# Performance work log

Hardware: AMD Instinct MI355X
Metric: run time of the kernel (lower is better)

Reference implementation:

```python
import jax, jax.numpy as jnp
import numpy as np

B, T, C, H = 8, 2048, 512, 512


def setup_inputs() -> dict:
    key = jax.random.key(0)
    ks = jax.random.split(key, 9)
    s = 1.0 / np.sqrt(C)
    return {
        "q": jax.random.normal(ks[0], (B, T, C), jnp.float32),
        "k": jax.random.normal(ks[1], (B, T, C), jnp.float32),
        "v": jax.random.normal(ks[2], (B, T, C), jnp.float32),
        "Wq": jax.random.normal(ks[3], (C, H), jnp.float32) * s,
        "bq": jax.random.normal(ks[4], (H,), jnp.float32) * 0.01,
        "Wk": jax.random.normal(ks[5], (C, H), jnp.float32) * s,
        "bk": jax.random.normal(ks[6], (H,), jnp.float32) * 0.01,
        "Wv": jax.random.normal(ks[7], (C, H), jnp.float32) * s,
        "bv": jax.random.normal(ks[8], (H,), jnp.float32) * 0.01,
    }


def reference(q, k, v, Wq, bq, Wk, bk, Wv, bv):
    # Linear projections (Real_Linear == nn.Linear): [B,T,C] @ [C,H] + [H]
    query = jnp.einsum('btc,ch->bth', q, Wq) + bq
    key_p = jnp.einsum('btc,ch->bth', k, Wk) + bk
    value = jnp.einsum('btc,ch->bth', v, Wv) + bv
    # energy = Q @ K^T / sqrt(H)  -> [B, T, T]
    energy = jnp.einsum('bth,byh->bty', query, key_p) / jnp.sqrt(jnp.asarray(H, query.dtype))
    attn = jax.nn.softmax(energy, axis=-1)
    # weighted value: [B, T, T] @ [B, T, H] -> [B, T, H]
    return jnp.einsum('bty,byh->bth', attn, value)
```

## Files before the change

### kernel.cpp

```cpp
#include <hip/hip_runtime.h>
#include <hip/hip_bf16.h>

typedef unsigned short u16;
typedef unsigned int u32;
typedef short s16x8 __attribute__((ext_vector_type(8)));
typedef float f32x4 __attribute__((ext_vector_type(4)));

#define NB 8
#define NT 2048
#define NC 512
#define NH 512

__device__ __forceinline__ u16 f2bf(float f) {
  unsigned u = __float_as_uint(f);
  u += 0x7FFFu + ((u >> 16) & 1u);
  return (u16)(u >> 16);
}

__device__ __forceinline__ void gld16(const u16* src, u16* lds_dst) {
  __builtin_amdgcn_global_load_lds(
      (const __attribute__((address_space(1))) u32*)src,
      (__attribute__((address_space(3))) u32*)lds_dst, 16, 0, 0);
}

__global__ __launch_bounds__(256) void wt_kernel(const float* __restrict__ Wq,
                                                 const float* __restrict__ Wk,
                                                 const float* __restrict__ Wv,
                                                 u16* __restrict__ WqT,
                                                 u16* __restrict__ WkT,
                                                 u16* __restrict__ WvT) {
  __shared__ float tile[32][33];
  const float* W = (blockIdx.z == 0) ? Wq : (blockIdx.z == 1) ? Wk : Wv;
  u16* WT = (blockIdx.z == 0) ? WqT : (blockIdx.z == 1) ? WkT : WvT;
  const int x = threadIdx.x & 31;
  const int y = threadIdx.x >> 5;
  const int k0 = blockIdx.x * 32, h0 = blockIdx.y * 32;
#pragma unroll
  for (int p = 0; p < 4; ++p)
    tile[y + 8 * p][x] = W[(size_t)(k0 + y + 8 * p) * NH + h0 + x];
  __syncthreads();
#pragma unroll
  for (int p = 0; p < 4; ++p)
    WT[(size_t)(h0 + y + 8 * p) * NC + k0 + x] = f2bf(tile[x][y + 8 * p]);
}

__global__ __launch_bounds__(256) void proj_kernel(const float* __restrict__ Xq,
                                                   const float* __restrict__ Xk,
                                                   const float* __restrict__ Xv,
                                                   const u16* __restrict__ WqT,
                                                   const u16* __restrict__ WkT,
                                                   const u16* __restrict__ WvT,
                                                   const float* __restrict__ bq,
                                                   const float* __restrict__ bk,
                                                   const float* __restrict__ bv,
                                                   u16* __restrict__ Yq,
                                                   u16* __restrict__ Yk,
                                                   u16* __restrict__ Yv) {
  __shared__ __align__(16) u16 Asub[2][128 * 40];
  __shared__ __align__(16) u16 Bsub[2][128 * 40];
  const int zz = blockIdx.z;
  const float* X = (zz == 0) ? Xq : (zz == 1) ? Xk : Xv;
  const u16* WT = (zz == 0) ? WqT : (zz == 1) ? WkT : WvT;
  const float* bias = (zz == 0) ? bq : (zz == 1) ? bk : bv;
  u16* Y = (zz == 0) ? Yq : (zz == 1) ? Yk : Yv;

  const int t = threadIdx.x;
  const int lane = t & 63;
  const int w = t >> 6;
  const int l16 = lane & 15;
  const int ko8 = (lane >> 4) * 8;
  const int m0 = blockIdx.y * 128;
  const int n0 = blockIdx.x * 128;
  const int wr = (w >> 1) * 64, wc = (w & 1) * 64;
  f32x4 acc[4][4] = {};

  float4 areg[4];
  int4 breg[2];
#define PLOAD(kt)                                                              \
  {                                                                            \
    const int k0_ = (kt) * 32;                                                 \
    _Pragma("unroll")                                                          \
    for (int p = 0; p < 4; ++p) {                                              \
      int c = t + 256 * p;                                                     \
      areg[p] = *(const float4*)&X[(size_t)(m0 + (c >> 3)) * NC + k0_ + (c & 7) * 4]; \
    }                                                                          \
    _Pragma("unroll")                                                          \
    for (int p = 0; p < 2; ++p) {                                              \
      int c = t + 256 * p;                                                     \
      breg[p] = *(const int4*)&WT[(size_t)(n0 + (c >> 2)) * NC + k0_ + (c & 3) * 8];  \
    }                                                                          \
  }
#define PWRITE(buf)                                                            \
  {                                                                            \
    _Pragma("unroll")                                                          \
    for (int p = 0; p < 4; ++p) {                                              \
      int c = t + 256 * p;                                                     \
      ushort4 bb;                                                              \
      bb.x = f2bf(areg[p].x); bb.y = f2bf(areg[p].y);                          \
      bb.z = f2bf(areg[p].z); bb.w = f2bf(areg[p].w);                          \
      *(ushort4*)&Asub[buf][(c >> 3) * 40 + (c & 7) * 4] = bb;                 \
    }                                                                          \
    _Pragma("unroll")                                                          \
    for (int p = 0; p < 2; ++p) {                                              \
      int c = t + 256 * p;                                                     \
      *(int4*)&Bsub[buf][(c >> 2) * 40 + (c & 3) * 8] = breg[p];               \
    }                                                                          \
  }

  PLOAD(0)
  PWRITE(0)
  __syncthreads();

  int pb = 0;
  for (int kt = 0; kt < 16; ++kt) {
    if (kt < 15) PLOAD(kt + 1)
    s16x8 af[4], bf[4];
#pragma unroll
    for (int i = 0; i < 4; ++i)
      af[i] = *(const s16x8*)&Asub[pb][(wr + i * 16 + l16) * 40 + ko8];
#pragma unroll
    for (int j = 0; j < 4; ++j)
      bf[j] = *(const s16x8*)&Bsub[pb][(wc + j * 16 + l16) * 40 + ko8];
#pragma unroll
    for (int i = 0; i < 4; ++i)
#pragma unroll
      for (int j = 0; j < 4; ++j)
        acc[i][j] = __builtin_amdgcn_mfma_f32_16x16x32_bf16(af[i], bf[j], acc[i][j], 0, 0, 0);
    if (kt < 15) PWRITE(pb ^ 1)
    __syncthreads();
    pb ^= 1;
  }
#undef PLOAD
#undef PWRITE
  const int rg = (lane >> 4) * 4;
#pragma unroll
  for (int i = 0; i < 4; ++i)
#pragma unroll
    for (int j = 0; j < 4; ++j) {
      const int col = n0 + wc + j * 16 + l16;
      const float bcol = bias[col];
#pragma unroll
      for (int jj = 0; jj < 4; ++jj) {
        const int row = m0 + wr + i * 16 + rg + jj;
        Y[(size_t)row * NH + col] = f2bf(acc[i][j][jj] + bcol);
      }
    }
}

__global__ __launch_bounds__(256) void vt_kernel(const u16* __restrict__ Vp,
                                                 u16* __restrict__ VpT) {
  __shared__ u16 tile[32][33];
  const int x = threadIdx.x & 31;
  const int y = threadIdx.x >> 5;
  const int t0 = blockIdx.x * 32, h0 = blockIdx.y * 32, b = blockIdx.z;
  const u16* src = Vp + (size_t)b * NT * NH;
  u16* dst = VpT + (size_t)b * NH * NT;
#pragma unroll
  for (int p = 0; p < 4; ++p)
    tile[y + 8 * p][x] = src[(size_t)(t0 + y + 8 * p) * NH + h0 + x];
  __syncthreads();
#pragma unroll
  for (int p = 0; p < 4; ++p)
    dst[(size_t)(h0 + y + 8 * p) * NT + t0 + x] = tile[x][y + 8 * p];
}

__global__ __launch_bounds__(512, 2) void flash_partial(const u16* __restrict__ Qp,
                                                        const u16* __restrict__ Kp,
                                                        const u16* __restrict__ VpT,
                                                        float* __restrict__ O0,
                                                        float* __restrict__ O1,
                                                        float* __restrict__ mlws) {
  __shared__ __align__(16) u16 Klds[2][32 * 512];
  __shared__ __align__(16) u16 Vlds[2][32 * 512];

  const int t = threadIdx.x;
  const int lane = t & 63;
  const int w = t >> 6;
  const int l16 = lane & 15;
  const int g = lane >> 4;
  const int g8 = g * 8;
  const int b = blockIdx.x;
  const int q0 = blockIdx.y * 128;
  const int z = blockIdx.z;
  const int qg = q0 + w * 16 + l16;
  const int kperm = (l16 >> 2) * 8 + (l16 & 3);
  const float kscale = 0.044194173824159216f;

  s16x8 qf[16];
  {
    const u16* qrow = Qp + (size_t)(b * NT + qg) * NH;
#pragma unroll
    for (int ks = 0; ks < 16; ++ks)
      qf[ks] = *(const s16x8*)&qrow[ks * 32 + g8];
  }

  f32x4 oacc[32] = {};
  float m_run = -1e30f, l_run = 0.f;

  const u16* kbat = Kp + (size_t)(b * NT + z * 1024) * NH;
  const u16* vbat = VpT + (size_t)b * NH * NT + z * 1024;

#define STAGE(buf, it)                                                         \
  {                                                                            \
    _Pragma("unroll")                                                          \
    for (int r = 0; r < 4; ++r) {                                              \
      const int i = w * 4 + r;                                      \
                 \
      gld16(kbat + (size_t)((it) * 32 + kperm + ((i & 1) << 2)) * NH           \
                 + ((i >> 1) << 5) + g8,                                       \
            &Klds[buf][i * 512]);                                              \
                                 \
      gld16(vbat + (size_t)(i * 16 + l16) * NT + (it) * 32 + g8,               \
            &Vlds[buf][i * 512]);                                              \
    }                                                                          \
  }

  STAGE(0, 0)
  __syncthreads();

  int pb = 0;
  for (int it = 0; it < 32; ++it) {
    if (it < 31) STAGE(pb ^ 1, it + 1)
    f32x4 s0 = {}, s1 = {};
    __builtin_amdgcn_s_setprio(1);
#pragma unroll
    for (int ks = 0; ks < 16; ++ks) {
      s16x8 kf0 = *(const s16x8*)&Klds[pb][(ks * 2 + 0) * 512 + lane * 8];
      s16x8 kf1 = *(const s16x8*)&Klds[pb][(ks * 2 + 1) * 512 + lane * 8];
      s0 = __builtin_amdgcn_mfma_f32_16x16x32_bf16(kf0, qf[ks], s0, 0, 0, 0);
      s1 = __builtin_amdgcn_mfma_f32_16x16x32_bf16(kf1, qf[ks], s1, 0, 0, 0);
    }
    __builtin_amdgcn_s_setprio(0);
    float pv[8];
#pragma unroll
    for (int j = 0; j < 4; ++j) { pv[j] = s0[j] * kscale; pv[4 + j] = s1[j] * kscale; }
    float mx = pv[0];
#pragma unroll
    for (int j = 1; j < 8; ++j) mx = fmaxf(mx, pv[j]);
    mx = fmaxf(mx, __shfl_xor(mx, 16, 64));
    mx = fmaxf(mx, __shfl_xor(mx, 32, 64));
    if (__any(mx > m_run + 8.f)) {
      const float m_new = fmaxf(m_run, mx);
      const float scale = __expf(m_run - m_new);
#pragma unroll
      for (int ht = 0; ht < 32; ++ht) {
        oacc[ht][0] *= scale; oacc[ht][1] *= scale;
        oacc[ht][2] *= scale; oacc[ht][3] *= scale;
      }
      l_run *= scale;
      m_run = m_new;
    }
    float ts = 0.f;
#pragma unroll
    for (int j = 0; j < 8; ++j) { pv[j] = __expf(pv[j] - m_run); ts += pv[j]; }
    l_run += ts;
    union { u32 u[4]; s16x8 v; } pf;
    pf.u[0] = ((u32)f2bf(pv[1]) << 16) | f2bf(pv[0]);
    pf.u[1] = ((u32)f2bf(pv[3]) << 16) | f2bf(pv[2]);
    pf.u[2] = ((u32)f2bf(pv[5]) << 16) | f2bf(pv[4]);
    pf.u[3] = ((u32)f2bf(pv[7]) << 16) | f2bf(pv[6]);
    __builtin_amdgcn_s_setprio(1);
#pragma unroll
    for (int ht = 0; ht < 32; ++ht) {
      s16x8 vf = *(const s16x8*)&Vlds[pb][ht * 512 + lane * 8];
      oacc[ht] = __builtin_amdgcn_mfma_f32_16x16x32_bf16(vf, pf.v, oacc[ht], 0, 0, 0);
    }
    __builtin_amdgcn_s_setprio(0);
    __syncthreads();
    pb ^= 1;
  }
  float* obase = (z ? O1 : O0) + (size_t)(b * NT + qg) * NH;
#pragma unroll
  for (int ht = 0; ht < 32; ++ht) {
    float4 st;
    st.x = oacc[ht][0]; st.y = oacc[ht][1];
    st.z = oacc[ht][2]; st.w = oacc[ht][3];
    *(float4*)&obase[ht * 16 + g * 4] = st;
  }
  float lt = l_run;
  lt += __shfl_xor(lt, 16, 64);
  lt += __shfl_xor(lt, 32, 64);
  if (g == 0) {
    const size_t row = (size_t)b * NT + qg;
    mlws[row * 4 + z * 2 + 0] = m_run;
    mlws[row * 4 + z * 2 + 1] = lt;
  }
#undef STAGE
}

__global__ __launch_bounds__(128) void merge_kernel(float* __restrict__ out,
                                                    const float* __restrict__ O1,
                                                    const float* __restrict__ mlws) {
  const size_t row = blockIdx.x;
  const float m0 = mlws[row * 4 + 0], l0 = mlws[row * 4 + 1];
  const float m1 = mlws[row * 4 + 2], l1 = mlws[row * 4 + 3];
  const float m = fmaxf(m0, m1);
  const float a0 = __expf(m0 - m), a1 = __expf(m1 - m);
  const float inv = 1.f / (a0 * l0 + a1 * l1);
  const float c0 = a0 * inv, c1 = a1 * inv;
  const size_t idx = row * NH + threadIdx.x * 4;
  float4 o0 = *(const float4*)&out[idx];
  float4 o1 = *(const float4*)&O1[idx];
  float4 r;
  r.x = c0 * o0.x + c1 * o1.x;
  r.y = c0 * o0.y + c1 * o1.y;
  r.z = c0 * o0.z + c1 * o1.z;
  r.w = c0 * o0.w + c1 * o1.w;
  *(float4*)&out[idx] = r;
}

__global__ __launch_bounds__(256, 1) void flash_kernel(const u16* __restrict__ Qp,
                                                       const u16* __restrict__ Kp,
                                                       const u16* __restrict__ VpT,
                                                       float* __restrict__ out) {
  __shared__ __align__(16) u16 Klds[2][32 * 512];
  __shared__ __align__(16) u16 Vlds[2][32 * 512];

  const int t = threadIdx.x;
  const int lane = t & 63;
  const int w = t >> 6;
  const int l16 = lane & 15;
  const int g = lane >> 4;
  const int g8 = g * 8;
  const int b = blockIdx.x;
  const int q0 = blockIdx.y * 64;
  const int qg = q0 + w * 16 + l16;
  const int kperm = (l16 >> 2) * 8 + (l16 & 3);
  const float kscale = 0.044194173824159216f;

  s16x8 qf[16];
  {
    const u16* qrow = Qp + (size_t)(b * NT + qg) * NH;
#pragma unroll
    for (int ks = 0; ks < 16; ++ks)
      qf[ks] = *(const s16x8*)&qrow[ks * 32 + g8];
  }
  f32x4 oacc[32] = {};
  float m_run = -1e30f, l_run = 0.f;
  const u16* kbat = Kp + (size_t)b * NT * NH;
  const u16* vbat = VpT + (size_t)b * NH * NT;

#pragma unroll
  for (int r = 0; r < 8; ++r) {
    const int i = w * 8 + r;
    gld16(kbat + (size_t)(kperm + ((i & 1) << 2)) * NH + ((i >> 1) << 5) + g8,
          &Klds[0][i * 512]);
    gld16(vbat + (size_t)(i * 16 + l16) * NT + g8, &Vlds[0][i * 512]);
  }
  __syncthreads();

  int pb = 0;
  for (int it = 0; it < 64; ++it) {
    if (it < 63) {
      const int kv1 = (it + 1) * 32;
      const int nb = pb ^ 1;
#pragma unroll
      for (int r = 0; r < 8; ++r) {
        const int i = w * 8 + r;
        gld16(kbat + (size_t)(kv1 + kperm + ((i & 1) << 2)) * NH + ((i >> 1) << 5) + g8,
              &Klds[nb][i * 512]);
        gld16(vbat + (size_t)(i * 16 + l16) * NT + kv1 + g8, &Vlds[nb][i * 512]);
      }
    }
    f32x4 s0 = {}, s1 = {};
#pragma unroll
    for (int ks = 0; ks < 16; ++ks) {
      s16x8 kf0 = *(const s16x8*)&Klds[pb][(ks * 2 + 0) * 512 + lane * 8];
      s16x8 kf1 = *(const s16x8*)&Klds[pb][(ks * 2 + 1) * 512 + lane * 8];
      s0 = __builtin_amdgcn_mfma_f32_16x16x32_bf16(kf0, qf[ks], s0, 0, 0, 0);
      s1 = __builtin_amdgcn_mfma_f32_16x16x32_bf16(kf1, qf[ks], s1, 0, 0, 0);
    }
    float pv[8];
#pragma unroll
    for (int j = 0; j < 4; ++j) { pv[j] = s0[j] * kscale; pv[4 + j] = s1[j] * kscale; }
    float mx = pv[0];
#pragma unroll
    for (int j = 1; j < 8; ++j) mx = fmaxf(mx, pv[j]);
    mx = fmaxf(mx, __shfl_xor(mx, 16, 64));
    mx = fmaxf(mx, __shfl_xor(mx, 32, 64));
    if (__any(mx > m_run + 8.f)) {
      const float m_new = fmaxf(m_run, mx);
      const float scale = __expf(m_run - m_new);
#pragma unroll
      for (int ht = 0; ht < 32; ++ht) {
        oacc[ht][0] *= scale; oacc[ht][1] *= scale;
        oacc[ht][2] *= scale; oacc[ht][3] *= scale;
      }
      l_run *= scale;
      m_run = m_new;
    }
    float ts = 0.f;
#pragma unroll
    for (int j = 0; j < 8; ++j) { pv[j] = __expf(pv[j] - m_run); ts += pv[j]; }
    l_run += ts;
    union { u32 u[4]; s16x8 v; } pf;
    pf.u[0] = ((u32)f2bf(pv[1]) << 16) | f2bf(pv[0]);
    pf.u[1] = ((u32)f2bf(pv[3]) << 16) | f2bf(pv[2]);
    pf.u[2] = ((u32)f2bf(pv[5]) << 16) | f2bf(pv[4]);
    pf.u[3] = ((u32)f2bf(pv[7]) << 16) | f2bf(pv[6]);
#pragma unroll
    for (int ht = 0; ht < 32; ++ht) {
      s16x8 vf = *(const s16x8*)&Vlds[pb][ht * 512 + lane * 8];
      oacc[ht] = __builtin_amdgcn_mfma_f32_16x16x32_bf16(vf, pf.v, oacc[ht], 0, 0, 0);
    }
    __syncthreads();
    pb ^= 1;
  }
  float lt = l_run;
  lt += __shfl_xor(lt, 16, 64);
  lt += __shfl_xor(lt, 32, 64);
  const float inv = 1.f / lt;
  float* obase = out + (size_t)(b * NT + qg) * NH;
#pragma unroll
  for (int ht = 0; ht < 32; ++ht) {
    float4 st;
    st.x = oacc[ht][0] * inv; st.y = oacc[ht][1] * inv;
    st.z = oacc[ht][2] * inv; st.w = oacc[ht][3] * inv;
    *(float4*)&obase[ht * 16 + g * 4] = st;
  }
}

extern "C" void kernel_launch(void* const* d_in, const int* in_sizes, int n_in,
                              void* d_out, int out_size, void* d_ws, size_t ws_size,
                              hipStream_t stream) {
  (void)in_sizes; (void)n_in; (void)out_size;
  const float* q  = (const float*)d_in[0];
  const float* k  = (const float*)d_in[1];
  const float* v  = (const float*)d_in[2];
  const float* Wq = (const float*)d_in[3];
  const float* bq = (const float*)d_in[4];
  const float* Wk = (const float*)d_in[5];
  const float* bk = (const float*)d_in[6];
  const float* Wv = (const float*)d_in[7];
  const float* bv = (const float*)d_in[8];
  float* out = (float*)d_out;

  u16* ws   = (u16*)d_ws;
  u16* WqT  = ws;
  u16* WkT  = WqT + (size_t)NC * NH;
  u16* WvT  = WkT + (size_t)NC * NH;
  u16* Qp   = WvT + (size_t)NC * NH;
  u16* Kp   = Qp + (size_t)NB * NT * NH;
  u16* Vp   = Kp + (size_t)NB * NT * NH;
  u16* VpT  = Vp + (size_t)NB * NT * NH;
  u16* endb = VpT + (size_t)NB * NT * NH;
  float* O1   = (float*)endb;
  float* mlws = O1 + (size_t)NB * NT * NH;
  const size_t need = (size_t)((char*)(mlws + (size_t)NB * NT * 4) - (char*)d_ws);

  wt_kernel<<<dim3(16, 16, 3), 256, 0, stream>>>(Wq, Wk, Wv, WqT, WkT, WvT);

  proj_kernel<<<dim3(4, 128, 3), 256, 0, stream>>>(q, k, v, WqT, WkT, WvT,
                                                   bq, bk, bv, Qp, Kp, Vp);

  vt_kernel<<<dim3(64, 16, NB), 256, 0, stream>>>(Vp, VpT);

  if (ws_size >= need) {
    flash_partial<<<dim3(NB, NT / 128, 2), 512, 0, stream>>>(Qp, Kp, VpT, out, O1, mlws);
    merge_kernel<<<dim3(NB * NT), 128, 0, stream>>>(out, O1, mlws);
  } else {
    flash_kernel<<<dim3(NB, NT / 64), 256, 0, stream>>>(Qp, Kp, VpT, out);
  }
}
```

Baseline: 214.7 us.

## Fuse V transpose into projection epilogue and split QK MFMA accumulation chains

The V projection now swaps the MFMA operand order so each lane holds a transposed accumulator fragment, and writes V directly into the transposed VpT layout, removing the separate vt_kernel launch and its round-trip through global memory. The flash kernel's QK^T loop now uses two independent accumulator chains per output tile, combined at the end, to shorten the dependent MFMA chain. The transposed store writes 16 consecutive t positions per h row, which is a less contiguous access pattern than before, and the extra accumulators raise register pressure.

```diff
diff --git a/kernel.cpp b/kernel.cpp
--- a/kernel.cpp
+++ b/kernel.cpp
@@ -55,14 +55,13 @@
                                                    const float* __restrict__ bv,
                                                    u16* __restrict__ Yq,
                                                    u16* __restrict__ Yk,
-                                                   u16* __restrict__ Yv) {
+                                                   u16* __restrict__ VpT) {
   __shared__ __align__(16) u16 Asub[2][128 * 40];
   __shared__ __align__(16) u16 Bsub[2][128 * 40];
   const int zz = blockIdx.z;
   const float* X = (zz == 0) ? Xq : (zz == 1) ? Xk : Xv;
   const u16* WT = (zz == 0) ? WqT : (zz == 1) ? WkT : WvT;
   const float* bias = (zz == 0) ? bq : (zz == 1) ? bk : bv;
-  u16* Y = (zz == 0) ? Yq : (zz == 1) ? Yk : Yv;
 
   const int t = threadIdx.x;
   const int lane = t & 63;
@@ -121,11 +120,19 @@
 #pragma unroll
     for (int j = 0; j < 4; ++j)
       bf[j] = *(const s16x8*)&Bsub[pb][(wc + j * 16 + l16) * 40 + ko8];
-#pragma unroll
-    for (int i = 0; i < 4; ++i)
-#pragma unroll
-      for (int j = 0; j < 4; ++j)
-        acc[i][j] = __builtin_amdgcn_mfma_f32_16x16x32_bf16(af[i], bf[j], acc[i][j], 0, 0, 0);
+    if (zz != 2) {
+#pragma unroll
+      for (int i = 0; i < 4; ++i)
+#pragma unroll
+        for (int j = 0; j < 4; ++j)
+          acc[i][j] = __builtin_amdgcn_mfma_f32_16x16x32_bf16(af[i], bf[j], acc[i][j], 0, 0, 0);
+    } else {
+#pragma unroll
+      for (int i = 0; i < 4; ++i)
+#pragma unroll
+        for (int j = 0; j < 4; ++j)
+          acc[i][j] = __builtin_amdgcn_mfma_f32_16x16x32_bf16(bf[j], af[i], acc[i][j], 0, 0, 0);
+    }
     if (kt < 15) PWRITE(pb ^ 1)
     __syncthreads();
     pb ^= 1;
@@ -133,35 +140,36 @@
 #undef PLOAD
 #undef PWRITE
   const int rg = (lane >> 4) * 4;
-#pragma unroll
-  for (int i = 0; i < 4; ++i)
-#pragma unroll
-    for (int j = 0; j < 4; ++j) {
-      const int col = n0 + wc + j * 16 + l16;
-      const float bcol = bias[col];
-#pragma unroll
-      for (int jj = 0; jj < 4; ++jj) {
-        const int row = m0 + wr + i * 16 + rg + jj;
-        Y[(size_t)row * NH + col] = f2bf(acc[i][j][jj] + bcol);
+  if (zz != 2) {
+    u16* Y = (zz == 0) ? Yq : Yk;
+#pragma unroll
+    for (int i = 0; i < 4; ++i)
+#pragma unroll
+      for (int j = 0; j < 4; ++j) {
+        const int col = n0 + wc + j * 16 + l16;
+        const float bcol = bias[col];
+#pragma unroll
+        for (int jj = 0; jj < 4; ++jj) {
+          const int row = m0 + wr + i * 16 + rg + jj;
+          Y[(size_t)row * NH + col] = f2bf(acc[i][j][jj] + bcol);
+        }
       }
-    }
-}
-
-__global__ __launch_bounds__(256) void vt_kernel(const u16* __restrict__ Vp,
-                                                 u16* __restrict__ VpT) {
-  __shared__ u16 tile[32][33];
-  const int x = threadIdx.x & 31;
-  const int y = threadIdx.x >> 5;
-  const int t0 = blockIdx.x * 32, h0 = blockIdx.y * 32, b = blockIdx.z;
-  const u16* src = Vp + (size_t)b * NT * NH;
-  u16* dst = VpT + (size_t)b * NH * NT;
-#pragma unroll
-  for (int p = 0; p < 4; ++p)
-    tile[y + 8 * p][x] = src[(size_t)(t0 + y + 8 * p) * NH + h0 + x];
-  __syncthreads();
-#pragma unroll
-  for (int p = 0; p < 4; ++p)
-    dst[(size_t)(h0 + y + 8 * p) * NT + t0 + x] = tile[x][y + 8 * p];
+  } else {
+    const int bidx = m0 >> 11;
+    u16* vbase = VpT + (size_t)bidx * NH * NT;
+#pragma unroll
+    for (int i = 0; i < 4; ++i) {
+      const int tcol = (m0 & 2047) + wr + i * 16 + l16;
+#pragma unroll
+      for (int j = 0; j < 4; ++j) {
+#pragma unroll
+        for (int jj = 0; jj < 4; ++jj) {
+          const int h = n0 + wc + j * 16 + rg + jj;
+          vbase[(size_t)h * NT + tcol] = f2bf(acc[i][j][jj] + bias[h]);
+        }
+      }
+    }
+  }
 }
 
 __global__ __launch_bounds__(512, 2) void flash_partial(const u16* __restrict__ Qp,
@@ -205,11 +213,9 @@
     _Pragma("unroll")                                                          \
     for (int r = 0; r < 4; ++r) {                                              \
       const int i = w * 4 + r;                                      \
-                 \
       gld16(kbat + (size_t)((it) * 32 + kperm + ((i & 1) << 2)) * NH           \
                  + ((i >> 1) << 5) + g8,                                       \
             &Klds[buf][i * 512]);                                              \
-                                 \
       gld16(vbat + (size_t)(i * 16 + l16) * NT + (it) * 32 + g8,               \
             &Vlds[buf][i * 512]);                                              \
     }                                                                          \
@@ -221,16 +227,22 @@
   int pb = 0;
   for (int it = 0; it < 32; ++it) {
     if (it < 31) STAGE(pb ^ 1, it + 1)
-    f32x4 s0 = {}, s1 = {};
+    f32x4 s0a = {}, s0b = {}, s1a = {}, s1b = {};
     __builtin_amdgcn_s_setprio(1);
 #pragma unroll
-    for (int ks = 0; ks < 16; ++ks) {
+    for (int ks = 0; ks < 8; ++ks) {
       s16x8 kf0 = *(const s16x8*)&Klds[pb][(ks * 2 + 0) * 512 + lane * 8];
       s16x8 kf1 = *(const s16x8*)&Klds[pb][(ks * 2 + 1) * 512 + lane * 8];
-      s0 = __builtin_amdgcn_mfma_f32_16x16x32_bf16(kf0, qf[ks], s0, 0, 0, 0);
-      s1 = __builtin_amdgcn_mfma_f32_16x16x32_bf16(kf1, qf[ks], s1, 0, 0, 0);
+      s16x8 kf2 = *(const s16x8*)&Klds[pb][((ks + 8) * 2 + 0) * 512 + lane * 8];
+      s16x8 kf3 = *(const s16x8*)&Klds[pb][((ks + 8) * 2 + 1) * 512 + lane * 8];
+      s0a = __builtin_amdgcn_mfma_f32_16x16x32_bf16(kf0, qf[ks], s0a, 0, 0, 0);
+      s1a = __builtin_amdgcn_mfma_f32_16x16x32_bf16(kf1, qf[ks], s1a, 0, 0, 0);
+      s0b = __builtin_amdgcn_mfma_f32_16x16x32_bf16(kf2, qf[ks + 8], s0b, 0, 0, 0);
+      s1b = __builtin_amdgcn_mfma_f32_16x16x32_bf16(kf3, qf[ks + 8], s1b, 0, 0, 0);
     }
     __builtin_amdgcn_s_setprio(0);
+    const f32x4 s0 = s0a + s0b;
+    const f32x4 s1 = s1a + s1b;
     float pv[8];
 #pragma unroll
     for (int j = 0; j < 4; ++j) { pv[j] = s0[j] * kscale; pv[4 + j] = s1[j] * kscale; }
@@ -451,9 +463,7 @@
   wt_kernel<<<dim3(16, 16, 3), 256, 0, stream>>>(Wq, Wk, Wv, WqT, WkT, WvT);
 
   proj_kernel<<<dim3(4, 128, 3), 256, 0, stream>>>(q, k, v, WqT, WkT, WvT,
-                                                   bq, bk, bv, Qp, Kp, Vp);
-
-  vt_kernel<<<dim3(64, 16, NB), 256, 0, stream>>>(Vp, VpT);
+                                                   bq, bk, bv, Qp, Kp, VpT);
 
   if (ws_size >= need) {
     flash_partial<<<dim3(NB, NT / 128, 2), 512, 0, stream>>>(Qp, Kp, VpT, out, O1, mlws);
```

After: 243.3 us. +13.3%, slower.
